# Kernel tuning notes

Measured on AMD Instinct MI355X. Metric: run time of the kernel, lower is better.

Reference implementation:

```python
import jax, jax.numpy as jnp
import numpy as np

D_MODEL = 512
N_HEADS = 8
D_HEAD = D_MODEL // N_HEADS
B = 8
N = 1024
EPS = 1e-5  # torch LayerNorm default


def setup_inputs() -> dict:
    key = jax.random.key(0)
    ks = jax.random.split(key, 12)
    x = jax.random.normal(ks[0], (B, N, D_MODEL), dtype=jnp.float32)
    adj = (jax.random.uniform(ks[1], (B, N, N)) < 0.05).astype(jnp.float32)
    s = 1.0 / np.sqrt(D_MODEL)
    def lin(kw, kb):
        W = jax.random.uniform(kw, (D_MODEL, D_MODEL), minval=-s, maxval=s, dtype=jnp.float32)
        b = jax.random.uniform(kb, (D_MODEL,), minval=-s, maxval=s, dtype=jnp.float32)
        return W, b
    Wq, bq = lin(ks[2], ks[3])
    Wk, bk = lin(ks[4], ks[5])
    Wv, bv = lin(ks[6], ks[7])
    Wo, bo = lin(ks[8], ks[9])
    gamma = jnp.ones((D_MODEL,), dtype=jnp.float32)
    beta = jnp.zeros((D_MODEL,), dtype=jnp.float32)
    return {"x": x, "adj": adj, "Wq": Wq, "bq": bq, "Wk": Wk, "bk": bk,
            "Wv": Wv, "bv": bv, "Wo": Wo, "bo": bo, "gamma": gamma, "beta": beta}


def reference(x, adj, Wq, bq, Wk, bk, Wv, bv, Wo, bo, gamma, beta):
    Bsz, n, _ = x.shape
    # QKV projections -> [b, h, n, d]
    def proj(W, b):
        y = x @ W.T + b
        return y.reshape(Bsz, n, N_HEADS, D_HEAD).transpose(0, 2, 1, 3)
    q, k, v = proj(Wq, bq), proj(Wk, bk), proj(Wv, bv)
    scores = jnp.einsum('bhqd,bhkd->bhqk', q, k) / np.sqrt(D_HEAD)
    # adjacency mask + self-loops, broadcast over heads
    mask = (adj + jnp.eye(n, dtype=adj.dtype)[None]) > 0  # [b, n, n]
    scores = jnp.where(mask[:, None], scores, -jnp.inf)
    attn = jax.nn.softmax(scores, axis=-1)  # dropout is identity in eval
    out = jnp.einsum('bhqk,bhkd->bhqd', attn, v)
    out = out.transpose(0, 2, 1, 3).reshape(Bsz, n, D_MODEL)
    out = out @ Wo.T + bo
    # residual + LayerNorm
    h = x + out
    mu = jnp.mean(h, axis=-1, keepdims=True)
    var = jnp.mean(jnp.square(h - mu), axis=-1, keepdims=True)
    return (h - mu) * jax.lax.rsqrt(var + EPS) * gamma + beta
```

## Files before the change

kernel.cpp:

```cpp
#include <hip/hip_runtime.h>

typedef __bf16 bf16;
typedef bf16 bf16x8 __attribute__((ext_vector_type(8)));
typedef bf16 bf16x4 __attribute__((ext_vector_type(4)));
typedef bf16 bf16x2 __attribute__((ext_vector_type(2)));
typedef float f32x4 __attribute__((ext_vector_type(4)));
typedef unsigned long long u64;
typedef unsigned int u32;

#define B_SZ 8
#define N_SEQ 1024
#define DMODEL 512
#define N_HEADS 8
#define D_HEAD 64
#define M_ROWS 8192

#define QSCALE 0.18033688011112042f

static constexpr size_t OFF_XB   = 0;
static constexpr size_t OFF_WQKV = (size_t)M_ROWS * DMODEL * 2;
static constexpr size_t OFF_WO   = OFF_WQKV + (size_t)1536 * 512 * 2;
static constexpr size_t OFF_BQKV = OFF_WO + (size_t)512 * 512 * 2;
static constexpr size_t OFF_Q    = OFF_BQKV + 1536 * 4;
static constexpr size_t OFF_K    = OFF_Q + (size_t)64 * 1024 * 64 * 2;
static constexpr size_t OFF_V    = OFF_K + (size_t)64 * 1024 * 64 * 2;
static constexpr size_t OFF_MASK = OFF_V + (size_t)64 * 1024 * 64 * 2;

#define PREP_X_BLK 4096
#define PREP_W_BLK 4102
#define PREP_M_BLK 32768

__device__ __forceinline__ f32x4 mfma16(bf16x8 a, bf16x8 b, f32x4 c) {
  return __builtin_amdgcn_mfma_f32_16x16x32_bf16(a, b, c, 0, 0, 0);
}

__device__ __forceinline__ int sidx(int row, int col) {
  return (row << 6) + (col ^ ((row & 7) << 3));
}

__device__ __forceinline__ void gload16(const void* g, void* l) {
  __builtin_amdgcn_global_load_lds(
      (const __attribute__((address_space(1))) void*)g,
      (__attribute__((address_space(3))) void*)l, 16, 0, 0);
}

__global__ void k_prep(const float* __restrict__ x, const float* __restrict__ adj,
                       const float* __restrict__ Wq, const float* __restrict__ Wk,
                       const float* __restrict__ Wv, const float* __restrict__ Wo,
                       const float* __restrict__ bq, const float* __restrict__ bk,
                       const float* __restrict__ bv,
                       bf16* __restrict__ xb, bf16* __restrict__ wqkv,
                       bf16* __restrict__ wo, float* __restrict__ bqkv,
                       u64* __restrict__ maskb) {
  int b = blockIdx.x;
  if (b < PREP_X_BLK) {
    int i = b * 256 + threadIdx.x;
    float4 v = reinterpret_cast<const float4*>(x)[i];
    bf16x4 o = { (bf16)v.x, (bf16)v.y, (bf16)v.z, (bf16)v.w };
    *reinterpret_cast<bf16x4*>(xb + (size_t)i * 4) = o;
  } else if (b < PREP_X_BLK + PREP_W_BLK) {
    int tid = (b - PREP_X_BLK) * 256 + threadIdx.x;
    if (tid < 1536 * 512) {
      int row = tid >> 9;
      const float* Wsrc = row < 512 ? Wq : row < 1024 ? Wk : Wv;
      wqkv[tid] = (bf16)Wsrc[((row & 511) << 9) | (tid & 511)];
    } else if (tid < 1536 * 512 + 512 * 512) {
      int t = tid - 1536 * 512;
      wo[t] = (bf16)Wo[t];
    } else if (tid < 1536 * 512 + 512 * 512 + 1536) {
      int t = tid - (1536 * 512 + 512 * 512);
      bqkv[t] = t < 512 ? bq[t] : t < 1024 ? bk[t - 512] : bv[t - 1024];
    }
  } else {
    int idx = (b - (PREP_X_BLK + PREP_W_BLK)) * 256 + threadIdx.x;
    int q = (idx >> 10) & 1023, k = idx & 1023;
    bool pred = (adj[idx] > 0.f) || (q == k);
    u64 bal = __ballot(pred);
    if ((threadIdx.x & 63) == 0) maskb[idx >> 6] = bal;
  }
}

__global__ __launch_bounds__(256) void k_gemm(const bf16* __restrict__ A,
    const bf16* __restrict__ W, int ncols, int mode,
    const float* __restrict__ bias, const float* __restrict__ xres,
    bf16* __restrict__ oq, bf16* __restrict__ okk, bf16* __restrict__ ov,
    bf16* __restrict__ oh) {
  __shared__ bf16 Al[128 * 64];
  __shared__ bf16 Bl[128 * 64];
  int nbx = ncols >> 7;
  int cpx = gridDim.x >> 3;
  int wid = (blockIdx.x & 7) * cpx + (blockIdx.x >> 3);
  int bx = wid % nbx, by = wid / nbx;
  int m0 = by << 7, n0 = bx << 7;
  int tid = threadIdx.x, lane = tid & 63, w = tid >> 6;
  int wr = (w >> 1) << 6, wc = (w & 1) << 6;
  int lrow = lane & 15, lg = lane >> 4, lko = lg * 8;
  int rl = lane >> 3;
  int csw = ((lane & 7) ^ rl) << 3;

  const bf16* Asrc = A + (size_t)(m0 + w * 32 + rl) * DMODEL + csw;
  const bf16* Wsrc = W + (size_t)(n0 + w * 32 + rl) * DMODEL + csw;
  bf16* Adst = &Al[(w * 4) * 512];
  bf16* Bdst = &Bl[(w * 4) * 512];

  f32x4 acc[4][4];
#pragma unroll
  for (int i = 0; i < 4; i++)
#pragma unroll
    for (int j = 0; j < 4; j++) acc[i][j] = f32x4{0.f, 0.f, 0.f, 0.f};

  for (int k0 = 0; k0 < DMODEL; k0 += 64) {
    __syncthreads();
#pragma unroll
    for (int i = 0; i < 4; i++) {
      gload16(Asrc + k0 + (size_t)i * 8 * DMODEL, Adst + i * 512);
      gload16(Wsrc + k0 + (size_t)i * 8 * DMODEL, Bdst + i * 512);
    }
    __syncthreads();

    bf16x8 afr[4][2], bfr[4][2];
#pragma unroll
    for (int i = 0; i < 4; i++) {
      afr[i][0] = *reinterpret_cast<const bf16x8*>(&Al[sidx(wr + i * 16 + lrow, lko)]);
      afr[i][1] = *reinterpret_cast<const bf16x8*>(&Al[sidx(wr + i * 16 + lrow, 32 + lko)]);
      bfr[i][0] = *reinterpret_cast<const bf16x8*>(&Bl[sidx(wc + i * 16 + lrow, lko)]);
      bfr[i][1] = *reinterpret_cast<const bf16x8*>(&Bl[sidx(wc + i * 16 + lrow, 32 + lko)]);
    }
#pragma unroll
    for (int i = 0; i < 4; i++)
#pragma unroll
      for (int j = 0; j < 4; j++) {
        acc[i][j] = mfma16(afr[i][0], bfr[j][0], acc[i][j]);
        acc[i][j] = mfma16(afr[i][1], bfr[j][1], acc[i][j]);
      }
  }

  int rbase = lg * 4;
  if (mode == 0) {
#pragma unroll
    for (int i = 0; i < 4; i++) {
      int row0 = m0 + wr + i * 16 + rbase;
#pragma unroll
      for (int j = 0; j < 4; j++) {
        int col = n0 + wc + j * 16 + lrow;
        int which = col >> 9, c2 = col & 511, hh = c2 >> 6, dd = c2 & 63;
        float bi = bias[col];
        if (which == 2) {
          int bb = row0 >> 10, nn = row0 & 1023;
          bf16x4 pack;
#pragma unroll
          for (int r = 0; r < 4; r++) pack[r] = (bf16)(acc[i][j][r] + bi);
          *reinterpret_cast<bf16x4*>(
              &ov[(((size_t)bb * N_HEADS + hh) * D_HEAD + dd) * N_SEQ + nn]) = pack;
        } else {
          bf16* dst = which == 0 ? oq : okk;
          float scl = which == 0 ? QSCALE : 1.0f;
#pragma unroll
          for (int r = 0; r < 4; r++) {
            int gm = row0 + r;
            int bb = gm >> 10, nn = gm & 1023;
            dst[(((size_t)bb * N_HEADS + hh) * N_SEQ + nn) * D_HEAD + dd] =
                (bf16)((acc[i][j][r] + bi) * scl);
          }
        }
      }
    }
  } else {
#pragma unroll
    for (int i = 0; i < 4; i++) {
      int row0 = m0 + wr + i * 16 + rbase;
#pragma unroll
      for (int j = 0; j < 4; j++) {
        int col = n0 + wc + j * 16 + lrow;
        float bi = bias[col];
#pragma unroll
        for (int r = 0; r < 4; r++) {
          int gm = row0 + r;
          float y = acc[i][j][r] + bi + xres[(size_t)gm * DMODEL + col];
          oh[(size_t)gm * DMODEL + col] = (bf16)y;
        }
      }
    }
  }
}

__global__ __launch_bounds__(256, 4) void k_attn(const bf16* __restrict__ Qb,
    const bf16* __restrict__ Kb, const bf16* __restrict__ Vtg,
    const u64* __restrict__ maskb, bf16* __restrict__ attn_out) {
  __shared__ bf16 Kl[2][64 * 64];
  __shared__ bf16 Vt[2][64 * 64];

  int bid = blockIdx.x;
  int work = ((bid & 7) << 7) | (bid >> 3);
  int bh = work >> 4, qb = work & 15;
  int bb = bh >> 3, hh = bh & 7;
  int tid = threadIdx.x, lane = tid & 63, w = tid >> 6;
  int lrow = lane & 15, lg = lane >> 4;
  int rl = lane >> 3;
  int csw = ((lane & 7) ^ rl) << 3;
  int q0w = qb * 64 + w * 16;

  const bf16* Qh = Qb + (size_t)bh * N_SEQ * D_HEAD;
  const bf16* Kh = Kb + (size_t)bh * N_SEQ * D_HEAD;
  const bf16* Vh = Vtg + (size_t)bh * D_HEAD * N_SEQ;
  const u32* m32 = (const u32*)(maskb + (size_t)bb * N_SEQ * 16);

  const bf16* Ksrc = Kh + (size_t)(w * 16 + rl) * D_HEAD + csw;
  const bf16* Vsrc = Vh + (size_t)(w * 16 + rl) * N_SEQ + csw;

  bf16x8 qf0 = *reinterpret_cast<const bf16x8*>(&Qh[(q0w + lrow) * 64 + lg * 8]);
  bf16x8 qf1 = *reinterpret_cast<const bf16x8*>(&Qh[(q0w + lrow) * 64 + 32 + lg * 8]);

  f32x4 o[4];
#pragma unroll
  for (int d = 0; d < 4; d++) o[d] = f32x4{0.f, 0.f, 0.f, 0.f};
  float ls = 0.f;

#define STAGE(buf, kt0)                                                     \
  {                                                                         \
    _Pragma("unroll") for (int i = 0; i < 2; i++) {                         \
      gload16(Ksrc + (size_t)(kt0) * 64 + i * 512, &Kl[buf][(w * 2 + i) * 512]); \
      gload16(Vsrc + (size_t)i * 8192 + (kt0), &Vt[buf][(w * 2 + i) * 512]);     \
    }                                                                       \
  }

  STAGE(0, 0);
  __syncthreads();
  int cur = 0;

  for (int kt = 0; kt < 16; kt++) {
    int kt0 = kt << 6;
    int midx = ((q0w + lrow) * 16 + kt) * 2;
    u32 mlo = m32[midx], mhi = m32[midx + 1];

    if (kt < 15) STAGE(cur ^ 1, kt0 + 64);

    f32x4 sc[4];
#pragma unroll
    for (int t = 0; t < 4; t++) {
      bf16x8 kf0 = *reinterpret_cast<const bf16x8*>(&Kl[cur][sidx(t * 16 + lrow, lg * 8)]);
      bf16x8 kf1 = *reinterpret_cast<const bf16x8*>(&Kl[cur][sidx(t * 16 + lrow, 32 + lg * 8)]);
      sc[t] = f32x4{0.f, 0.f, 0.f, 0.f};
      __builtin_amdgcn_s_setprio(1);
      sc[t] = mfma16(kf0, qf0, sc[t]);
      sc[t] = mfma16(kf1, qf1, sc[t]);
      __builtin_amdgcn_s_setprio(0);
    }

    bf16x8 pa[2];
#pragma unroll
    for (int m = 0; m < 2; m++) {
      u32 mw = m == 0 ? mlo : mhi;
#pragma unroll
      for (int j = 0; j < 8; j++) {
        int sh = ((j >> 2) << 4) + lg * 4 + (j & 3);
        int t = 2 * m + (j >> 2), r = j & 3;
        bool bit = (mw >> sh) & 1u;
        float pv = bit ? exp2f(sc[t][r]) : 0.f;
        ls += pv;
        pa[m][j] = (bf16)pv;
      }
    }

#pragma unroll
    for (int d = 0; d < 4; d++) {
#pragma unroll
      for (int m = 0; m < 2; m++) {
        bf16x4 va = *reinterpret_cast<const bf16x4*>(
            &Vt[cur][sidx(d * 16 + lrow, m * 32 + lg * 4)]);
        bf16x4 vb = *reinterpret_cast<const bf16x4*>(
            &Vt[cur][sidx(d * 16 + lrow, m * 32 + 16 + lg * 4)]);
        bf16x8 vf = {va[0], va[1], va[2], va[3], vb[0], vb[1], vb[2], vb[3]};
        __builtin_amdgcn_s_setprio(1);
        o[d] = mfma16(vf, pa[m], o[d]);
        __builtin_amdgcn_s_setprio(0);
      }
    }

    __syncthreads();
    cur ^= 1;
  }

  ls += __shfl_xor(ls, 16);
  ls += __shfl_xor(ls, 32);
  float inv = 1.f / ls;

  int gq = q0w + lrow;
#pragma unroll
  for (int d = 0; d < 4; d++) {
    bf16x4 pk;
#pragma unroll
    for (int r = 0; r < 4; r++) pk[r] = (bf16)(o[d][r] * inv);
    *reinterpret_cast<bf16x4*>(
        &attn_out[((size_t)(bb * N_SEQ + gq)) * DMODEL + hh * 64 + d * 16 + lg * 4]) = pk;
  }
#undef STAGE
}

__global__ __launch_bounds__(256) void k_ln(const bf16* __restrict__ hb,
    const float* __restrict__ gamma, const float* __restrict__ beta,
    float* __restrict__ out) {
  int row = blockIdx.x, tid = threadIdx.x;
  bf16x2 v2 = *reinterpret_cast<const bf16x2*>(hb + (size_t)row * DMODEL + tid * 2);
  float vx = (float)v2[0], vy = (float)v2[1];
  float s = vx + vy, ss = vx * vx + vy * vy;
#pragma unroll
  for (int off = 1; off < 64; off <<= 1) {
    s += __shfl_xor(s, off);
    ss += __shfl_xor(ss, off);
  }
  __shared__ float as_[4], ass_[4];
  int w = tid >> 6;
  if ((tid & 63) == 0) { as_[w] = s; ass_[w] = ss; }
  __syncthreads();
  s = as_[0] + as_[1] + as_[2] + as_[3];
  ss = ass_[0] + ass_[1] + ass_[2] + ass_[3];
  float mu = s * (1.f / 512.f);
  float var = ss * (1.f / 512.f) - mu * mu;
  float rstd = rsqrtf(var + 1e-5f);
  float2 g = reinterpret_cast<const float2*>(gamma)[tid];
  float2 bt = reinterpret_cast<const float2*>(beta)[tid];
  float2 o;
  o.x = (vx - mu) * rstd * g.x + bt.x;
  o.y = (vy - mu) * rstd * g.y + bt.y;
  reinterpret_cast<float2*>(out + (size_t)row * DMODEL)[tid] = o;
}

extern "C" void kernel_launch(void* const* d_in, const int* in_sizes, int n_in,
                              void* d_out, int out_size, void* d_ws, size_t ws_size,
                              hipStream_t stream) {
  const float* x     = (const float*)d_in[0];
  const float* adj   = (const float*)d_in[1];
  const float* Wq    = (const float*)d_in[2];
  const float* bq    = (const float*)d_in[3];
  const float* Wk    = (const float*)d_in[4];
  const float* bk    = (const float*)d_in[5];
  const float* Wv    = (const float*)d_in[6];
  const float* bv    = (const float*)d_in[7];
  const float* Wo    = (const float*)d_in[8];
  const float* bo    = (const float*)d_in[9];
  const float* gamma = (const float*)d_in[10];
  const float* beta  = (const float*)d_in[11];

  char* ws = (char*)d_ws;
  bf16* xb    = (bf16*)(ws + OFF_XB);
  bf16* wqkv  = (bf16*)(ws + OFF_WQKV);
  bf16* wo    = (bf16*)(ws + OFF_WO);
  float* bqkv = (float*)(ws + OFF_BQKV);
  bf16* Qb    = (bf16*)(ws + OFF_Q);
  bf16* Kb    = (bf16*)(ws + OFF_K);
  bf16* Vb    = (bf16*)(ws + OFF_V);
  u64* maskb  = (u64*)(ws + OFF_MASK);
  bf16* attn  = xb;
  bf16* hb    = (bf16*)(ws + OFF_Q);
  float* out  = (float*)d_out;

  k_prep<<<dim3(PREP_X_BLK + PREP_W_BLK + PREP_M_BLK), dim3(256), 0, stream>>>(
      x, adj, Wq, Wk, Wv, Wo, bq, bk, bv, xb, wqkv, wo, bqkv, maskb);

  k_gemm<<<dim3((M_ROWS / 128) * (1536 / 128)), dim3(256), 0, stream>>>(
      xb, wqkv, 1536, 0, bqkv, nullptr, Qb, Kb, Vb, nullptr);

  k_attn<<<dim3(1024), dim3(256), 0, stream>>>(Qb, Kb, Vb, maskb, attn);

  k_gemm<<<dim3((M_ROWS / 128) * (512 / 128)), dim3(256), 0, stream>>>(
      attn, wo, 512, 1, bo, x, nullptr, nullptr, nullptr, hb);

  k_ln<<<dim3(M_ROWS), dim3(256), 0, stream>>>(hb, gamma, beta, out);
}
```

Measured before the change: 105.7 us.

## Preload mask bits into registers and hand-schedule K/V double-buffer waits in attention

```diff
diff --git a/kernel.cpp b/kernel.cpp
--- a/kernel.cpp
+++ b/kernel.cpp
@@ -208,6 +208,12 @@
   const bf16* Ksrc = Kh + (size_t)(w * 16 + rl) * D_HEAD + csw;
   const bf16* Vsrc = Vh + (size_t)(w * 16 + rl) * N_SEQ + csw;
 
+  const u32* mp = m32 + (size_t)(q0w + lrow) * 32;
+  u32 mk[32];
+#pragma unroll
+  for (int i = 0; i < 8; i++)
+    *reinterpret_cast<uint4*>(&mk[i * 4]) = reinterpret_cast<const uint4*>(mp)[i];
+
   bf16x8 qf0 = *reinterpret_cast<const bf16x8*>(&Qh[(q0w + lrow) * 64 + lg * 8]);
   bf16x8 qf1 = *reinterpret_cast<const bf16x8*>(&Qh[(q0w + lrow) * 64 + 32 + lg * 8]);
 
@@ -225,15 +231,29 @@
   }
 
   STAGE(0, 0);
-  __syncthreads();
-  int cur = 0;
-
+  asm volatile("s_waitcnt vmcnt(0)" ::: "memory");
+  __builtin_amdgcn_sched_barrier(0);
+  __builtin_amdgcn_s_barrier();
+  __builtin_amdgcn_sched_barrier(0);
+
+#pragma unroll
   for (int kt = 0; kt < 16; kt++) {
-    int kt0 = kt << 6;
-    int midx = ((q0w + lrow) * 16 + kt) * 2;
-    u32 mlo = m32[midx], mhi = m32[midx + 1];
-
-    if (kt < 15) STAGE(cur ^ 1, kt0 + 64);
+    const int cur = kt & 1;
+    u32 mlo = mk[kt * 2], mhi = mk[kt * 2 + 1];
+
+    if (kt < 15) {
+      STAGE(cur ^ 1, (kt + 1) << 6);
+      __builtin_amdgcn_sched_barrier(0);
+      asm volatile("s_waitcnt vmcnt(4)" ::: "memory");
+      __builtin_amdgcn_sched_barrier(0);
+      __builtin_amdgcn_s_barrier();
+      __builtin_amdgcn_sched_barrier(0);
+    } else {
+      asm volatile("s_waitcnt vmcnt(0)" ::: "memory");
+      __builtin_amdgcn_sched_barrier(0);
+      __builtin_amdgcn_s_barrier();
+      __builtin_amdgcn_sched_barrier(0);
+    }
 
     f32x4 sc[4];
 #pragma unroll
@@ -277,8 +297,11 @@
       }
     }
 
-    __syncthreads();
-    cur ^= 1;
+    if (kt < 15) {
+      __builtin_amdgcn_sched_barrier(0);
+      __builtin_amdgcn_s_barrier();
+      __builtin_amdgcn_sched_barrier(0);
+    }
   }
 
   ls += __shfl_xor(ls, 16);
```

After: 201.6 us. 1.91x slower.

## Process two query sub-tiles per wave in attention and permute V layout

Applied to the files above, without the earlier changes.

```diff
diff --git a/kernel.cpp b/kernel.cpp
--- a/kernel.cpp
+++ b/kernel.cpp
@@ -147,11 +147,12 @@
         float bi = bias[col];
         if (which == 2) {
           int bb = row0 >> 10, nn = row0 & 1023;
+          int n2 = (nn & ~63) | (nn & 32) | ((nn & 12) << 1) | ((nn & 16) >> 2);
           bf16x4 pack;
 #pragma unroll
           for (int r = 0; r < 4; r++) pack[r] = (bf16)(acc[i][j][r] + bi);
           *reinterpret_cast<bf16x4*>(
-              &ov[(((size_t)bb * N_HEADS + hh) * D_HEAD + dd) * N_SEQ + nn]) = pack;
+              &ov[(((size_t)bb * N_HEADS + hh) * D_HEAD + dd) * N_SEQ + n2]) = pack;
         } else {
           bf16* dst = which == 0 ? oq : okk;
           float scl = which == 0 ? QSCALE : 1.0f;
@@ -184,7 +185,7 @@
   }
 }
 
-__global__ __launch_bounds__(256, 4) void k_attn(const bf16* __restrict__ Qb,
+__global__ __launch_bounds__(128, 2) void k_attn(const bf16* __restrict__ Qb,
     const bf16* __restrict__ Kb, const bf16* __restrict__ Vtg,
     const u64* __restrict__ maskb, bf16* __restrict__ attn_out) {
   __shared__ bf16 Kl[2][64 * 64];
@@ -198,30 +199,36 @@
   int lrow = lane & 15, lg = lane >> 4;
   int rl = lane >> 3;
   int csw = ((lane & 7) ^ rl) << 3;
-  int q0w = qb * 64 + w * 16;
+  int q0w = qb * 64 + w * 32;
 
   const bf16* Qh = Qb + (size_t)bh * N_SEQ * D_HEAD;
   const bf16* Kh = Kb + (size_t)bh * N_SEQ * D_HEAD;
   const bf16* Vh = Vtg + (size_t)bh * D_HEAD * N_SEQ;
   const u32* m32 = (const u32*)(maskb + (size_t)bb * N_SEQ * 16);
 
-  const bf16* Ksrc = Kh + (size_t)(w * 16 + rl) * D_HEAD + csw;
-  const bf16* Vsrc = Vh + (size_t)(w * 16 + rl) * N_SEQ + csw;
-
-  bf16x8 qf0 = *reinterpret_cast<const bf16x8*>(&Qh[(q0w + lrow) * 64 + lg * 8]);
-  bf16x8 qf1 = *reinterpret_cast<const bf16x8*>(&Qh[(q0w + lrow) * 64 + 32 + lg * 8]);
-
-  f32x4 o[4];
-#pragma unroll
-  for (int d = 0; d < 4; d++) o[d] = f32x4{0.f, 0.f, 0.f, 0.f};
-  float ls = 0.f;
-
-#define STAGE(buf, kt0)                                                     \
-  {                                                                         \
-    _Pragma("unroll") for (int i = 0; i < 2; i++) {                         \
-      gload16(Ksrc + (size_t)(kt0) * 64 + i * 512, &Kl[buf][(w * 2 + i) * 512]); \
-      gload16(Vsrc + (size_t)i * 8192 + (kt0), &Vt[buf][(w * 2 + i) * 512]);     \
-    }                                                                       \
+  const bf16* Ksrc = Kh + (size_t)(w * 32 + rl) * D_HEAD + csw;
+  const bf16* Vsrc = Vh + (size_t)(w * 32 + rl) * N_SEQ + csw;
+
+  bf16x8 qf[2][2];
+#pragma unroll
+  for (int s = 0; s < 2; s++) {
+    qf[s][0] = *reinterpret_cast<const bf16x8*>(&Qh[(q0w + s * 16 + lrow) * 64 + lg * 8]);
+    qf[s][1] = *reinterpret_cast<const bf16x8*>(&Qh[(q0w + s * 16 + lrow) * 64 + 32 + lg * 8]);
+  }
+
+  f32x4 o[2][4];
+#pragma unroll
+  for (int s = 0; s < 2; s++)
+#pragma unroll
+    for (int d = 0; d < 4; d++) o[s][d] = f32x4{0.f, 0.f, 0.f, 0.f};
+  float ls[2] = {0.f, 0.f};
+
+#define STAGE(buf, kt0)                                                        \
+  {                                                                            \
+    _Pragma("unroll") for (int i = 0; i < 4; i++) {                            \
+      gload16(Ksrc + (size_t)(kt0) * 64 + i * 8 * 64, &Kl[buf][(w * 4 + i) * 512]); \
+      gload16(Vsrc + (kt0) + (size_t)i * 8 * N_SEQ, &Vt[buf][(w * 4 + i) * 512]);   \
+    }                                                                          \
   }
 
   STAGE(0, 0);
@@ -230,49 +237,57 @@
 
   for (int kt = 0; kt < 16; kt++) {
     int kt0 = kt << 6;
-    int midx = ((q0w + lrow) * 16 + kt) * 2;
-    u32 mlo = m32[midx], mhi = m32[midx + 1];
+    u32 ml[2], mh[2];
+#pragma unroll
+    for (int s = 0; s < 2; s++) {
+      int midx = ((q0w + s * 16 + lrow) * 16 + kt) * 2;
+      ml[s] = m32[midx];
+      mh[s] = m32[midx + 1];
+    }
 
     if (kt < 15) STAGE(cur ^ 1, kt0 + 64);
 
-    f32x4 sc[4];
+    f32x4 sc[2][4];
 #pragma unroll
     for (int t = 0; t < 4; t++) {
       bf16x8 kf0 = *reinterpret_cast<const bf16x8*>(&Kl[cur][sidx(t * 16 + lrow, lg * 8)]);
       bf16x8 kf1 = *reinterpret_cast<const bf16x8*>(&Kl[cur][sidx(t * 16 + lrow, 32 + lg * 8)]);
-      sc[t] = f32x4{0.f, 0.f, 0.f, 0.f};
       __builtin_amdgcn_s_setprio(1);
-      sc[t] = mfma16(kf0, qf0, sc[t]);
-      sc[t] = mfma16(kf1, qf1, sc[t]);
+#pragma unroll
+      for (int s = 0; s < 2; s++) {
+        sc[s][t] = f32x4{0.f, 0.f, 0.f, 0.f};
+        sc[s][t] = mfma16(kf0, qf[s][0], sc[s][t]);
+        sc[s][t] = mfma16(kf1, qf[s][1], sc[s][t]);
+      }
       __builtin_amdgcn_s_setprio(0);
     }
 
-    bf16x8 pa[2];
-#pragma unroll
-    for (int m = 0; m < 2; m++) {
-      u32 mw = m == 0 ? mlo : mhi;
-#pragma unroll
-      for (int j = 0; j < 8; j++) {
-        int sh = ((j >> 2) << 4) + lg * 4 + (j & 3);
-        int t = 2 * m + (j >> 2), r = j & 3;
-        bool bit = (mw >> sh) & 1u;
-        float pv = bit ? exp2f(sc[t][r]) : 0.f;
-        ls += pv;
-        pa[m][j] = (bf16)pv;
-      }
-    }
+    bf16x8 pa[2][2];
+#pragma unroll
+    for (int s = 0; s < 2; s++)
+#pragma unroll
+      for (int m = 0; m < 2; m++) {
+        u32 mw = m == 0 ? ml[s] : mh[s];
+#pragma unroll
+        for (int j = 0; j < 8; j++) {
+          int sh = ((j >> 2) << 4) + lg * 4 + (j & 3);
+          int t = 2 * m + (j >> 2), r = j & 3;
+          bool bit = (mw >> sh) & 1u;
+          float pv = bit ? exp2f(sc[s][t][r]) : 0.f;
+          ls[s] += pv;
+          pa[s][m][j] = (bf16)pv;
+        }
+      }
 
 #pragma unroll
     for (int d = 0; d < 4; d++) {
 #pragma unroll
       for (int m = 0; m < 2; m++) {
-        bf16x4 va = *reinterpret_cast<const bf16x4*>(
-            &Vt[cur][sidx(d * 16 + lrow, m * 32 + lg * 4)]);
-        bf16x4 vb = *reinterpret_cast<const bf16x4*>(
-            &Vt[cur][sidx(d * 16 + lrow, m * 32 + 16 + lg * 4)]);
-        bf16x8 vf = {va[0], va[1], va[2], va[3], vb[0], vb[1], vb[2], vb[3]};
+        bf16x8 vf = *reinterpret_cast<const bf16x8*>(
+            &Vt[cur][sidx(d * 16 + lrow, m * 32 + lg * 8)]);
         __builtin_amdgcn_s_setprio(1);
-        o[d] = mfma16(vf, pa[m], o[d]);
+        o[0][d] = mfma16(vf, pa[0][m], o[0][d]);
+        o[1][d] = mfma16(vf, pa[1][m], o[1][d]);
         __builtin_amdgcn_s_setprio(0);
       }
     }
@@ -281,18 +296,24 @@
     cur ^= 1;
   }
 
-  ls += __shfl_xor(ls, 16);
-  ls += __shfl_xor(ls, 32);
-  float inv = 1.f / ls;
-
-  int gq = q0w + lrow;
-#pragma unroll
-  for (int d = 0; d < 4; d++) {
-    bf16x4 pk;
-#pragma unroll
-    for (int r = 0; r < 4; r++) pk[r] = (bf16)(o[d][r] * inv);
-    *reinterpret_cast<bf16x4*>(
-        &attn_out[((size_t)(bb * N_SEQ + gq)) * DMODEL + hh * 64 + d * 16 + lg * 4]) = pk;
+#pragma unroll
+  for (int s = 0; s < 2; s++) {
+    ls[s] += __shfl_xor(ls[s], 16);
+    ls[s] += __shfl_xor(ls[s], 32);
+  }
+
+#pragma unroll
+  for (int s = 0; s < 2; s++) {
+    float inv = 1.f / ls[s];
+    int gq = q0w + s * 16 + lrow;
+#pragma unroll
+    for (int d = 0; d < 4; d++) {
+      bf16x4 pk;
+#pragma unroll
+      for (int r = 0; r < 4; r++) pk[r] = (bf16)(o[s][d][r] * inv);
+      *reinterpret_cast<bf16x4*>(
+          &attn_out[((size_t)(bb * N_SEQ + gq)) * DMODEL + hh * 64 + d * 16 + lg * 4]) = pk;
+    }
   }
 #undef STAGE
 }
@@ -361,7 +382,7 @@
   k_gemm<<<dim3((M_ROWS / 128) * (1536 / 128)), dim3(256), 0, stream>>>(
       xb, wqkv, 1536, 0, bqkv, nullptr, Qb, Kb, Vb, nullptr);
 
-  k_attn<<<dim3(1024), dim3(256), 0, stream>>>(Qb, Kb, Vb, maskb, attn);
+  k_attn<<<dim3(1024), dim3(128), 0, stream>>>(Qb, Kb, Vb, maskb, attn);
 
   k_gemm<<<dim3((M_ROWS / 128) * (512 / 128)), dim3(256), 0, stream>>>(
       attn, wo, 512, 1, bo, x, nullptr, nullptr, nullptr, hb);
```

Measured after the change: 117.7 us. 1.11x slower.
